# Performance work log

Hardware: AMD Instinct MI355X
Metric: run time of the kernel (lower is better)

Reference implementation:

```python
import jax, jax.numpy as jnp
import numpy as np

B, D, K = 65536, 128, 8
BOUND = 3.0
MIN_BIN_W = 1e-3   # min_bin_width
MIN_BIN_H = 1e-3   # min_bin_height
MIN_DERIV = 1e-3   # min_derivative
EPS = 1e-6


def setup_inputs() -> dict:
    key = jax.random.key(0)
    k1, k2, k3, k4 = jax.random.split(key, 4)
    return {
        "x": jax.random.normal(k1, (B, D), jnp.float32) * 1.5,
        "unnormalized_widths": jax.random.normal(k2, (D, K), jnp.float32),
        "unnormalized_heights": jax.random.normal(k3, (D, K), jnp.float32),
        "unnormalized_derivatives": jax.random.normal(k4, (D, K - 1), jnp.float32),
    }


def _calculate_knots(lengths, lower, upper):
    # lengths: [D, K] summing to ~1 -> scaled lengths and knot positions [D, K+1]
    knots = jnp.cumsum(lengths, axis=-1)
    knots = jnp.pad(knots, ((0, 0), (1, 0)))
    knots = (upper - lower) * knots + lower
    knots = knots.at[..., 0].set(lower)
    knots = knots.at[..., -1].set(upper)
    return knots[..., 1:] - knots[..., :-1], knots


def _select_bins(p, idx):
    # p: [D, Kp] per-dim tables, idx: [B, D] bin indices -> [B, D]
    i = jnp.clip(idx, 0, p.shape[-1] - 1)
    return p[jnp.arange(p.shape[0])[None, :], i]


def _spline_forward(x, uw, uh, ud):
    w = jax.nn.softmax(uw, axis=-1)
    h = jax.nn.softmax(uh, axis=-1)
    d = jax.nn.softplus(ud)

    num_bins = w.shape[-1]
    widths = MIN_BIN_W + (1.0 - MIN_BIN_W * num_bins) * w
    heights = MIN_BIN_H + (1.0 - MIN_BIN_H * num_bins) * h
    derivs = jnp.pad(MIN_DERIV + d, ((0, 0), (1, 1)), constant_values=1.0 - MIN_DERIV)  # [D, K+1]

    widths, cumwidths = _calculate_knots(widths, -BOUND, BOUND)
    heights, cumheights = _calculate_knots(heights, -BOUND, BOUND)

    inside = (x >= -BOUND) & (x <= BOUND)
    xc = jnp.clip(x, -BOUND, BOUND)  # keep tail values finite; masked out below

    # searchsorted: which bin each input falls into   [B, D]
    bin_idx = jnp.sum(xc[..., None] >= (cumwidths + EPS)[None, :, :], axis=-1) - 1

    iw = _select_bins(widths, bin_idx)
    icw = _select_bins(cumwidths, bin_idx)
    ich = _select_bins(cumheights, bin_idx)
    idelta = _select_bins(heights / widths, bin_idx)
    id0 = _select_bins(derivs, bin_idx)
    id1 = _select_bins(derivs[..., 1:], bin_idx)
    ih = _select_bins(heights, bin_idx)

    # rational quadratic spline (forward)
    theta = (xc - icw) / iw
    t1m = theta * (1.0 - theta)
    numerator = ih * (idelta * theta ** 2 + id0 * t1m)
    denominator = idelta + (id0 + id1 - 2.0 * idelta) * t1m
    out = ich + numerator / denominator
    dnum = idelta ** 2 * (id1 * theta ** 2 + 2.0 * idelta * t1m + id0 * (1.0 - theta) ** 2)
    lad = jnp.log(dnum) - 2.0 * jnp.log(denominator)

    u = jnp.where(inside, out, x)          # identity outside tail bound
    lad = jnp.where(inside, lad, 0.0)
    return u, lad


def reference(x, unnormalized_widths, unnormalized_heights, unnormalized_derivatives):
    u, lad = _spline_forward(x, unnormalized_widths, unnormalized_heights, unnormalized_derivatives)
    log_detJ = jnp.sum(lad, axis=1)
    return u, log_detJ
```

## Files before the change

kernel.cpp:

```cpp
#include <hip/hip_runtime.h>
#include <math.h>

namespace {
constexpr int D = 128;
constexpr int K = 8;
constexpr float BOUND = 3.0f;
constexpr float EPS = 1e-6f;
constexpr float MIN_BIN_W = 1e-3f;
constexpr float MIN_BIN_H = 1e-3f;
constexpr float MIN_DERIV = 1e-3f;
constexpr int STRIDE = 63;
constexpr int WPB = 4;
}

__global__ __launch_bounds__(256) void spline_fwd(
    const float* __restrict__ x,
    const float* __restrict__ uw,
    const float* __restrict__ uh,
    const float* __restrict__ ud,
    float* __restrict__ out_u,
    float* __restrict__ out_ld,
    int nrows)
{
    __shared__ float s_tab[D * STRIDE];

    const int tid = threadIdx.x;
    if (tid < D) {
        const int d = tid;
        float wv[K], hv[K], cw[K + 1], ch[K + 1], der[K + 1];

        {
            const float* p = uw + d * K;
            float m = p[0];
            #pragma unroll
            for (int j = 1; j < K; ++j) m = fmaxf(m, p[j]);
            float s = 0.f;
            #pragma unroll
            for (int j = 0; j < K; ++j) { wv[j] = __expf(p[j] - m); s += wv[j]; }
            const float inv = 1.f / s;
            #pragma unroll
            for (int j = 0; j < K; ++j)
                wv[j] = MIN_BIN_W + (1.f - MIN_BIN_W * K) * (wv[j] * inv);
        }
        {
            const float* p = uh + d * K;
            float m = p[0];
            #pragma unroll
            for (int j = 1; j < K; ++j) m = fmaxf(m, p[j]);
            float s = 0.f;
            #pragma unroll
            for (int j = 0; j < K; ++j) { hv[j] = __expf(p[j] - m); s += hv[j]; }
            const float inv = 1.f / s;
            #pragma unroll
            for (int j = 0; j < K; ++j)
                hv[j] = MIN_BIN_H + (1.f - MIN_BIN_H * K) * (hv[j] * inv);
        }
        cw[0] = -BOUND; ch[0] = -BOUND;
        float cs_w = 0.f, cs_h = 0.f;
        #pragma unroll
        for (int j = 0; j < K; ++j) {
            cs_w += wv[j]; cw[j + 1] = 2.f * BOUND * cs_w - BOUND;
            cs_h += hv[j]; ch[j + 1] = 2.f * BOUND * cs_h - BOUND;
        }
        cw[K] = BOUND; ch[K] = BOUND;

        der[0] = 1.f - MIN_DERIV;
        der[K] = 1.f - MIN_DERIV;
        {
            const float* p = ud + d * (K - 1);
            #pragma unroll
            for (int j = 1; j < K; ++j) {
                const float v = p[j - 1];
                const float sp = log1pf(__expf(-fabsf(v))) + fmaxf(v, 0.f);
                der[j] = MIN_DERIV + sp;
            }
        }

        float* row = s_tab + d * STRIDE;
        #pragma unroll
        for (int j = 0; j < K; ++j) {
            const float w = cw[j + 1] - cw[j];
            const float h = ch[j + 1] - ch[j];
            row[j * 7 + 0] = 1.f / w;
            row[j * 7 + 1] = cw[j];
            row[j * 7 + 2] = ch[j];
            row[j * 7 + 3] = h / w;
            row[j * 7 + 4] = der[j];
            row[j * 7 + 5] = der[j + 1];
            row[j * 7 + 6] = h;
        }
        #pragma unroll
        for (int j = 0; j < K - 1; ++j) row[56 + j] = cw[j + 1];
    }
    __syncthreads();

    const int wave = tid >> 6;
    const int lane = tid & 63;
    const int rstep = gridDim.x * WPB;

    for (int r = blockIdx.x * WPB + wave; r < nrows; r += rstep) {
        const float* xr = x + (size_t)r * D;
        float* ur = out_u + (size_t)r * D;
        float lacc = 0.f;
        #pragma unroll
        for (int half = 0; half < 2; ++half) {
            const int d = lane + half * 64;
            const float xv = xr[d];
            const bool inside = (xv >= -BOUND) & (xv <= BOUND);
            const float xc = fminf(fmaxf(xv, -BOUND), BOUND);
            const float* row = s_tab + d * STRIDE;

            int idx = 0;
            #pragma unroll
            for (int j = 0; j < K - 1; ++j)
                idx += (xc >= row[56 + j] + EPS) ? 1 : 0;

            const float* t = row + idx * 7;
            const float inv_w = t[0];
            const float icw   = t[1];
            const float ich   = t[2];
            const float dl    = t[3];
            const float d0    = t[4];
            const float d1    = t[5];
            const float ih    = t[6];

            const float theta = (xc - icw) * inv_w;
            const float omt   = 1.f - theta;
            const float t1m   = theta * omt;
            const float th2   = theta * theta;
            const float num   = ih * (dl * th2 + d0 * t1m);
            const float den   = dl + (d0 + d1 - 2.f * dl) * t1m;
            const float outv  = ich + __fdividef(num, den);
            const float dnum  = dl * dl * (d1 * th2 + 2.f * dl * t1m + d0 * omt * omt);
            const float lad   = __logf(dnum) - 2.f * __logf(den);

            ur[d] = inside ? outv : xv;
            lacc += inside ? lad : 0.f;
        }
        #pragma unroll
        for (int off = 32; off > 0; off >>= 1)
            lacc += __shfl_down(lacc, off);
        if (lane == 0) out_ld[r] = lacc;
    }
}

extern "C" void kernel_launch(void* const* d_in, const int* in_sizes, int n_in,
                              void* d_out, int out_size, void* d_ws, size_t ws_size,
                              hipStream_t stream) {
    const float* x  = (const float*)d_in[0];
    const float* uw = (const float*)d_in[1];
    const float* uh = (const float*)d_in[2];
    const float* ud = (const float*)d_in[3];
    const int nrows = in_sizes[0] / D;
    float* out_u  = (float*)d_out;
    float* out_ld = (float*)d_out + (size_t)nrows * D;
    spline_fwd<<<1280, 256, 0, stream>>>(x, uw, uh, ud, out_u, out_ld, nrows);
}
```

Baseline: 110.0 us.

## Pad spline table to 8-float records, cache knots in registers, vector LDS loads

The per-dimension spline table is re-laid-out into 8-float aligned records per bin, so each lookup takes two float4 LDS reads instead of seven scalar ones. The combined derivative term is precomputed, and the EPS-shifted knot thresholds are hoisted into registers once per thread rather than read from shared memory on every row. The grid is reduced from 1280 to 1024 blocks. This adds register pressure, and the 68-float stride may cause LDS bank conflicts on the float4 reads.

```diff
diff --git a/kernel.cpp b/kernel.cpp
--- a/kernel.cpp
+++ b/kernel.cpp
@@ -9,8 +9,31 @@
 constexpr float MIN_BIN_W = 1e-3f;
 constexpr float MIN_BIN_H = 1e-3f;
 constexpr float MIN_DERIV = 1e-3f;
-constexpr int STRIDE = 63;
+constexpr int REC = 8;
+constexpr int S = K * REC + 4;
 constexpr int WPB = 4;
+}
+
+__device__ __forceinline__ float spline_one(float xv, const float* __restrict__ row,
+                                            const float* kn, float* __restrict__ outp) {
+    const bool inside = (xv >= -BOUND) & (xv <= BOUND);
+    const float xc = fminf(fmaxf(xv, -BOUND), BOUND);
+    int idx = 0;
+    #pragma unroll
+    for (int j = 0; j < 7; ++j) idx += (xc >= kn[j]) ? 1 : 0;
+    const float4 ra = *(const float4*)(row + idx * REC);
+    const float4 rb = *(const float4*)(row + idx * REC + 4);
+    const float theta = (xc - ra.x) * ra.y;
+    const float omt   = 1.f - theta;
+    const float t1m   = theta * omt;
+    const float th2   = theta * theta;
+    const float num   = rb.y * (ra.w * th2 + ra.z * t1m);
+    const float den   = ra.w + rb.w * t1m;
+    const float outv  = rb.x + __fdividef(num, den);
+    const float dnum  = ra.w * ra.w * (rb.z * th2 + 2.f * ra.w * t1m + ra.z * omt * omt);
+    const float lad   = __logf(dnum) - 2.f * __logf(den);
+    *outp = inside ? outv : xv;
+    return inside ? lad : 0.f;
 }
 
 __global__ __launch_bounds__(256) void spline_fwd(
@@ -22,7 +45,7 @@
     float* __restrict__ out_ld,
     int nrows)
 {
-    __shared__ float s_tab[D * STRIDE];
+    __shared__ __align__(16) float s_tab[D * S];
 
     const int tid = threadIdx.x;
     if (tid < D) {
@@ -76,67 +99,46 @@
             }
         }
 
-        float* row = s_tab + d * STRIDE;
+        float* row = s_tab + d * S;
         #pragma unroll
         for (int j = 0; j < K; ++j) {
-            const float w = cw[j + 1] - cw[j];
-            const float h = ch[j + 1] - ch[j];
-            row[j * 7 + 0] = 1.f / w;
-            row[j * 7 + 1] = cw[j];
-            row[j * 7 + 2] = ch[j];
-            row[j * 7 + 3] = h / w;
-            row[j * 7 + 4] = der[j];
-            row[j * 7 + 5] = der[j + 1];
-            row[j * 7 + 6] = h;
+            const float w  = cw[j + 1] - cw[j];
+            const float h  = ch[j + 1] - ch[j];
+            const float dl = h / w;
+            row[j * REC + 0] = cw[j];
+            row[j * REC + 1] = 1.f / w;
+            row[j * REC + 2] = der[j];
+            row[j * REC + 3] = dl;
+            row[j * REC + 4] = ch[j];
+            row[j * REC + 5] = h;
+            row[j * REC + 6] = der[j + 1];
+            row[j * REC + 7] = der[j] + der[j + 1] - 2.f * dl;
         }
-        #pragma unroll
-        for (int j = 0; j < K - 1; ++j) row[56 + j] = cw[j + 1];
     }
     __syncthreads();
 
     const int wave = tid >> 6;
     const int lane = tid & 63;
+    const int da = lane;
+    const int db = lane + 64;
+    const float* rowa = s_tab + da * S;
+    const float* rowb = s_tab + db * S;
+
+    float kna[7], knb[7];
+    #pragma unroll
+    for (int j = 0; j < 7; ++j) {
+        kna[j] = rowa[(j + 1) * REC] + EPS;
+        knb[j] = rowb[(j + 1) * REC] + EPS;
+    }
+
     const int rstep = gridDim.x * WPB;
-
     for (int r = blockIdx.x * WPB + wave; r < nrows; r += rstep) {
         const float* xr = x + (size_t)r * D;
         float* ur = out_u + (size_t)r * D;
-        float lacc = 0.f;
-        #pragma unroll
-        for (int half = 0; half < 2; ++half) {
-            const int d = lane + half * 64;
-            const float xv = xr[d];
-            const bool inside = (xv >= -BOUND) & (xv <= BOUND);
-            const float xc = fminf(fmaxf(xv, -BOUND), BOUND);
-            const float* row = s_tab + d * STRIDE;
-
-            int idx = 0;
-            #pragma unroll
-            for (int j = 0; j < K - 1; ++j)
-                idx += (xc >= row[56 + j] + EPS) ? 1 : 0;
-
-            const float* t = row + idx * 7;
-            const float inv_w = t[0];
-            const float icw   = t[1];
-            const float ich   = t[2];
-            const float dl    = t[3];
-            const float d0    = t[4];
-            const float d1    = t[5];
-            const float ih    = t[6];
-
-            const float theta = (xc - icw) * inv_w;
-            const float omt   = 1.f - theta;
-            const float t1m   = theta * omt;
-            const float th2   = theta * theta;
-            const float num   = ih * (dl * th2 + d0 * t1m);
-            const float den   = dl + (d0 + d1 - 2.f * dl) * t1m;
-            const float outv  = ich + __fdividef(num, den);
-            const float dnum  = dl * dl * (d1 * th2 + 2.f * dl * t1m + d0 * omt * omt);
-            const float lad   = __logf(dnum) - 2.f * __logf(den);
-
-            ur[d] = inside ? outv : xv;
-            lacc += inside ? lad : 0.f;
-        }
+        const float xa = xr[da];
+        const float xb = xr[db];
+        float lacc = spline_one(xa, rowa, kna, ur + da)
+                   + spline_one(xb, rowb, knb, ur + db);
         #pragma unroll
         for (int off = 32; off > 0; off >>= 1)
             lacc += __shfl_down(lacc, off);
@@ -154,5 +156,5 @@
     const int nrows = in_sizes[0] / D;
     float* out_u  = (float*)d_out;
     float* out_ld = (float*)d_out + (size_t)nrows * D;
-    spline_fwd<<<1280, 256, 0, stream>>>(x, uw, uh, ud, out_u, out_ld, nrows);
+    spline_fwd<<<1024, 256, 0, stream>>>(x, uw, uh, ud, out_u, out_ld, nrows);
 }
```

New measurement: 103.2 us. 6.2% less time.
